# Kernel tuning notes

Hardware: AMD Instinct MI355X
Metric: run time of the kernel (lower is better)

## Reference

```python
import jax, jax.numpy as jnp
import numpy as np
from jax import lax

B, L, D_MODEL = 4, 1024, 512
D_STATE, D_CONV, D_INNER = 16, 4, 2 * D_MODEL


def setup_inputs() -> dict:
    key = jax.random.key(0)
    ks = jax.random.split(key, 8)
    s = 0.02
    x = jax.random.normal(ks[0], (B, L, D_MODEL), dtype=jnp.float32)
    W_in = jax.random.normal(ks[1], (D_MODEL, 2 * D_INNER), dtype=jnp.float32) * s
    conv_w = jax.random.normal(ks[2], (D_INNER, 1, D_CONV), dtype=jnp.float32) * s  # OIH, depthwise
    conv_b = jnp.zeros((D_INNER,), jnp.float32)
    W_x = jax.random.normal(ks[3], (D_INNER, 2 * D_STATE), dtype=jnp.float32) * s
    W_dt = jax.random.normal(ks[4], (D_INNER, D_INNER), dtype=jnp.float32) * s
    b_dt = jnp.zeros((D_INNER,), jnp.float32)
    # A_log = -logspace(log10(0.001), log10(1.0), d_state); used directly as A in the scan
    A_log = -jnp.logspace(np.log10(1e-3), 0.0, D_STATE, dtype=jnp.float32)
    D_skip = jnp.ones((D_INNER,), jnp.float32) * 0.1
    W_out = jax.random.normal(ks[5], (D_INNER, D_MODEL), dtype=jnp.float32) * s
    gamma = jnp.ones((D_MODEL,), jnp.float32)
    beta = jnp.zeros((D_MODEL,), jnp.float32)
    return dict(x=x, W_in=W_in, conv_w=conv_w, conv_b=conv_b, W_x=W_x, W_dt=W_dt,
                b_dt=b_dt, A_log=A_log, D_skip=D_skip, W_out=W_out, gamma=gamma, beta=beta)


def _mamba_forward(x, W_in, conv_w, conv_b, W_x, W_dt, b_dt, A_log, D_skip, W_out, gamma, beta):
    x = jnp.clip(x, -10.0, 10.0)
    x_and_res = x @ W_in                                  # [B, L, 2*d_inner]
    xp, res = jnp.split(x_and_res, 2, axis=-1)
    # Depthwise causal conv1d: torch pads d_conv-1 both sides then slices [:L] -> left-pad only.
    xt = jnp.transpose(xp, (0, 2, 1))                     # [B, d_inner, L]
    xc = lax.conv_general_dilated(xt, conv_w, window_strides=(1,),
                                  padding=[(D_CONV - 1, 0)],
                                  dimension_numbers=('NCH', 'OIH', 'NCH'),
                                  feature_group_count=D_INNER)
    xc = xc + conv_b[None, :, None]
    xc = jax.nn.silu(jnp.transpose(xc, (0, 2, 1)))        # [B, L, d_inner]
    ssm = xc @ W_x                                        # [B, L, 2*d_state]
    Bm, Cm = jnp.split(ssm, 2, axis=-1)                   # each [B, L, d_state]
    delta = xc @ W_dt + b_dt                              # [B, L, d_inner] (no softplus in source)

    # Selective scan over time (sequential recurrence)
    def step(h, inp):
        u_t, d_t, B_t, C_t = inp                          # [B,I], [B,I], [B,S], [B,S]
        dA = jnp.exp(jnp.clip(d_t[:, :, None] * A_log, -5.0, 5.0))   # [B, I, S]
        h = dA * h + (d_t[:, :, None] * B_t[:, None, :]) * u_t[:, :, None]
        y = jnp.einsum('bis,bs->bi', h, C_t)
        return h, y

    tm = lambda a: jnp.swapaxes(a, 0, 1)                  # time-major
    h0 = jnp.zeros((x.shape[0], D_INNER, D_STATE), xc.dtype)
    _, ys = lax.scan(step, h0, (tm(xc), tm(delta), tm(Bm), tm(Cm)))
    y = jnp.swapaxes(ys, 0, 1) + xc * D_skip              # D skip connection

    y = y * jax.nn.silu(res)                              # gating
    out = y @ W_out
    r = out + x                                           # residual
    mu = jnp.mean(r, axis=-1, keepdims=True)
    var = jnp.var(r, axis=-1, keepdims=True)
    return gamma * (r - mu) / jnp.sqrt(var + 1e-5) + beta


def reference(x, W_in, conv_w, conv_b, W_x, W_dt, b_dt, A_log, D_skip, W_out, gamma, beta):
    return _mamba_forward(x, W_in, conv_w, conv_b, W_x, W_dt, b_dt, A_log, D_skip, W_out, gamma, beta)
```

## Files before the change

kernel.cpp:

```cpp
#include <hip/hip_runtime.h>
#include <hip/hip_bf16.h>

typedef __hip_bfloat16 bf16;
typedef unsigned short ushort_t;
typedef unsigned int uint_t;
typedef __attribute__((ext_vector_type(8))) __bf16 bf16x8;
typedef __attribute__((ext_vector_type(8))) ushort_t u16x8;
typedef __attribute__((ext_vector_type(4))) ushort_t u16x4;
typedef __attribute__((ext_vector_type(4))) float f32x4;
typedef __attribute__((ext_vector_type(2))) float f32x2;

#define BB 4
#define LL 1024
#define DM 512
#define DS 16
#define DI 1024
#define ROWS 4096
#define NC 64
#define CT 16
#define NDTX 1152

__device__ __forceinline__ float b2f(bf16 v) { return __bfloat162float(v); }

__device__ __forceinline__ float load_flag(const void* src, int i, int isbf)
{
    return isbf ? b2f(((const bf16*)src)[i]) : ((const float*)src)[i];
}

__device__ __forceinline__ ushort_t f2b_bits(float v)
{
    bf16 t = __float2bfloat16(v);
    return *(ushort_t*)&t;
}

__device__ __forceinline__ float bits2f(ushort_t u)
{
    uint_t w = ((uint_t)u) << 16;
    return __uint_as_float(w);
}

__device__ __forceinline__ int detect_local(const ushort_t* wdt)
{
    __shared__ int bad;
    if (threadIdx.x == 0) bad = 0;
    __syncthreads();
    ushort_t u = wdt[threadIdx.x & 255];
    if (((u >> 7) & 0xFF) >= 127) atomicAdd(&bad, 1);
    __syncthreads();
    return (bad <= 8) ? 1 : 0;
}

__global__ __launch_bounds__(256)
void prep_all(const void* x, const void* Win, const void* Wdt, const void* Wx,
              const void* Wout, const void* cw, const void* cb, const void* Alog,
              const void* Dsk, const void* gam, const void* bet, const void* bdtin,
              bf16* __restrict__ xbf, bf16* __restrict__ WtIn,
              bf16* __restrict__ WtDtx, bf16* __restrict__ WtOut,
              float* __restrict__ ccw, float* __restrict__ ccb,
              float* __restrict__ cAlg, float* __restrict__ cDsk,
              float* __restrict__ cgam, float* __restrict__ cbet,
              float* __restrict__ bdtx)
{
    const int isbf = detect_local((const ushort_t*)Wdt);
    int blk = blockIdx.x;

    if (blk < 2048) {
        int idx = blk * 256 + threadIdx.x;
        float v[4];
        if (isbf) {
            uint2 raw = ((const uint2*)x)[idx];
            v[0] = __uint_as_float(raw.x << 16);
            v[1] = __uint_as_float(raw.x & 0xFFFF0000u);
            v[2] = __uint_as_float(raw.y << 16);
            v[3] = __uint_as_float(raw.y & 0xFFFF0000u);
        } else {
            float4 raw = ((const float4*)x)[idx];
            v[0] = raw.x; v[1] = raw.y; v[2] = raw.z; v[3] = raw.w;
        }
        uint_t b0, b1;
        b0 = f2b_bits(fminf(fmaxf(v[0], -10.f), 10.f))
           | ((uint_t)f2b_bits(fminf(fmaxf(v[1], -10.f), 10.f)) << 16);
        b1 = f2b_bits(fminf(fmaxf(v[2], -10.f), 10.f))
           | ((uint_t)f2b_bits(fminf(fmaxf(v[3], -10.f), 10.f)) << 16);
        uint2 ow; ow.x = b0; ow.y = b1;
        ((uint2*)xbf)[idx] = ow;
    } else if (blk < 4640) {
        int tb = blk - 2048;
        const void* src; bf16* dst; int K, Nsrc, tpr;
        if (tb < 1024)      { src = Win;  dst = WtIn;   K = 512;  Nsrc = 2048; tpr = 64; }
        else if (tb < 2048) { tb -= 1024; src = Wdt;  dst = WtDtx; K = 1024; Nsrc = 1024; tpr = 32; }
        else if (tb < 2080) { tb -= 2048; src = Wx;   dst = WtDtx + 1024 * 1024; K = 1024; Nsrc = 32; tpr = 1; }
        else                { tb -= 2080; src = Wout; dst = WtOut;  K = 1024; Nsrc = 512;  tpr = 16; }
        int k0 = (tb / tpr) * 32, n0 = (tb % tpr) * 32;

        __shared__ float tile[32][33];
        int tx = threadIdx.x & 31, ty = threadIdx.x >> 5;
        #pragma unroll
        for (int j = 0; j < 4; ++j)
            tile[ty + 8 * j][tx] = load_flag(src, (k0 + ty + 8 * j) * Nsrc + n0 + tx, isbf);
        __syncthreads();
        #pragma unroll
        for (int j = 0; j < 4; ++j)
            dst[(size_t)(n0 + ty + 8 * j) * K + k0 + tx] = __float2bfloat16(tile[tx][ty + 8 * j]);
    } else {
        int i = (blk - 4640) * 256 + threadIdx.x;
        if (i < 4096)        ccw[i] = load_flag(cw, i, isbf);
        else if (i < 5120)   ccb[i - 4096] = load_flag(cb, i - 4096, isbf);
        else if (i < 5136)   cAlg[i - 5120] = load_flag(Alog, i - 5120, isbf);
        else if (i < 6160)   cDsk[i - 5136] = load_flag(Dsk, i - 5136, isbf);
        else if (i < 6672)   cgam[i - 6160] = load_flag(gam, i - 6160, isbf);
        else if (i < 7184)   cbet[i - 6672] = load_flag(bet, i - 6672, isbf);
        else if (i < 8336) {
            int j = i - 7184;
            bdtx[j] = (j < DI) ? load_flag(bdtin, j, isbf) : 0.f;
        } else if (i < 106640) {
            (WtDtx + 1056 * 1024)[i - 8336] = __float2bfloat16(0.f);
        }
    }
}

__device__ __forceinline__ void gload16(const bf16* g, ushort_t* l)
{
    __builtin_amdgcn_global_load_lds(
        (const __attribute__((address_space(1))) void*)g,
        (__attribute__((address_space(3))) void*)l, 16, 0, 0);
}

template <int TM, int TN, bool OBF, bool OT, bool SPLIT>
__global__ __launch_bounds__(256)
void gemm_mfma(const bf16* __restrict__ A, const bf16* __restrict__ Bt,
               const float* __restrict__ bias, void* __restrict__ Cv,
               void* __restrict__ Cv2, int M, int N, int K)
{
    constexpr int MI = TM / 32, NJ = TN / 32;
    constexpr int NQA = TM * 8 / 256;
    constexpr int NQB = TN * 8 / 256;
    __shared__ ushort_t As[TM * 64];
    __shared__ ushort_t Bs[TN * 64];

    const int tid = threadIdx.x;
    const int lane = tid & 63;
    const int w = tid >> 6;
    const int wr = w >> 1, wc = w & 1;
    const int m0 = blockIdx.y * TM;
    const int n0 = blockIdx.x * TN;

    const bf16* gA[NQA]; ushort_t* lA[NQA];
    #pragma unroll
    for (int q = 0; q < NQA; ++q) {
        int p = q * 256 + tid;
        int row = p >> 3, kc = ((p & 7) - row) & 7;
        gA[q] = A + (size_t)(m0 + row) * K + kc * 8;
        lA[q] = &As[(q * 256 + w * 64) * 8];
    }
    const bf16* gB[NQB]; ushort_t* lB[NQB];
    #pragma unroll
    for (int q = 0; q < NQB; ++q) {
        int p = q * 256 + tid;
        int row = p >> 3, kc = ((p & 7) - row) & 7;
        gB[q] = Bt + (size_t)(n0 + row) * K + kc * 8;
        lB[q] = &Bs[(q * 256 + w * 64) * 8];
    }

    f32x4 acc[MI][NJ];
    #pragma unroll
    for (int i = 0; i < MI; ++i)
        #pragma unroll
        for (int j = 0; j < NJ; ++j)
            acc[i][j] = (f32x4){0.f, 0.f, 0.f, 0.f};

    const int ko = lane >> 4;
    const int ml = lane & 15;

    for (int k0 = 0; k0 < K; k0 += 64) {
        #pragma unroll
        for (int q = 0; q < NQA; ++q) gload16(gA[q] + k0, lA[q]);
        #pragma unroll
        for (int q = 0; q < NQB; ++q) gload16(gB[q] + k0, lB[q]);
        __syncthreads();

        #pragma unroll
        for (int half = 0; half < 2; ++half) {
            bf16x8 af[MI], bfr[NJ];
            #pragma unroll
            for (int i = 0; i < MI; ++i) {
                int m = wr * (TM / 2) + i * 16 + ml;
                af[i] = *(const bf16x8*)&As[(m * 8 + ((half * 4 + ko + m) & 7)) * 8];
            }
            #pragma unroll
            for (int j = 0; j < NJ; ++j) {
                int n = wc * (TN / 2) + j * 16 + ml;
                bfr[j] = *(const bf16x8*)&Bs[(n * 8 + ((half * 4 + ko + n) & 7)) * 8];
            }
            #pragma unroll
            for (int i = 0; i < MI; ++i)
                #pragma unroll
                for (int j = 0; j < NJ; ++j)
                    acc[i][j] = __builtin_amdgcn_mfma_f32_16x16x32_bf16(
                        af[i], bfr[j], acc[i][j], 0, 0, 0);
        }
        __syncthreads();
    }

    const int rq = lane >> 4;
    #pragma unroll
    for (int j = 0; j < NJ; ++j) {
        int n = n0 + wc * (TN / 2) + j * 16 + ml;
        float bv = bias ? bias[n] : 0.f;
        #pragma unroll
        for (int i = 0; i < MI; ++i) {
            int mb = m0 + wr * (TM / 2) + i * 16 + rq * 4;
            if (SPLIT && n >= 1024) {
                if (n < 1088) {
                    #pragma unroll
                    for (int r = 0; r < 4; ++r)
                        ((bf16*)Cv2)[(size_t)(mb + r) * 64 + (n - 1024)] =
                            __float2bfloat16(acc[i][j][r] + bv);
                }
            } else if (OT) {
                u16x4 pk;
                #pragma unroll
                for (int r = 0; r < 4; ++r)
                    pk[r] = f2b_bits(acc[i][j][r] + bv);
                *(u16x4*)((ushort_t*)Cv + (size_t)n * M + mb) = pk;
            } else {
                #pragma unroll
                for (int r = 0; r < 4; ++r) {
                    float v = acc[i][j][r] + bv;
                    if (OBF) ((bf16*)Cv)[(size_t)(mb + r) * N + n] = __float2bfloat16(v);
                    else     ((float*)Cv)[(size_t)(mb + r) * N + n] = v;
                }
            }
        }
    }
}

__global__ __launch_bounds__(256)
void conv_silu(const bf16* __restrict__ xrbT, const float* __restrict__ cw,
               const float* __restrict__ cb, bf16* __restrict__ xcT,
               bf16* __restrict__ xc)
{
    __shared__ ushort_t tile[64 * 72];
    const int blk = blockIdx.x;
    const int ch0 = (blk & 15) * 64;
    const int T0b = (blk >> 4) * 64;
    const int lc = threadIdx.x >> 2, tg = threadIdx.x & 3;
    const int i = ch0 + lc;
    const int T0 = T0b + tg * 16;

    const ushort_t* base = (const ushort_t*)xrbT + (size_t)i * ROWS + T0;
    u16x8 m0 = *(const u16x8*)base;
    u16x8 m1 = *(const u16x8*)(base + 8);
    u16x8 pv = {0, 0, 0, 0, 0, 0, 0, 0};
    if ((T0 & (LL - 1)) != 0) pv = *(const u16x8*)(base - 8);

    float4 w = ((const float4*)cw)[i];
    float bs = cb[i];
    float xm3 = bits2f(pv[5]), xm2 = bits2f(pv[6]), xm1 = bits2f(pv[7]);
    u16x8 o0, o1;
    #pragma unroll
    for (int tt = 0; tt < 16; ++tt) {
        float x0 = bits2f(tt < 8 ? m0[tt] : m1[tt - 8]);
        float acc = bs;
        acc = fmaf(xm3, w.x, acc);
        acc = fmaf(xm2, w.y, acc);
        acc = fmaf(xm1, w.z, acc);
        acc = fmaf(x0,  w.w, acc);
        ushort_t ob = f2b_bits(acc / (1.f + __expf(-acc)));
        if (tt < 8) o0[tt] = ob; else o1[tt - 8] = ob;
        xm3 = xm2; xm2 = xm1; xm1 = x0;
    }
    ushort_t* dt = (ushort_t*)xcT + (size_t)i * ROWS + T0;
    *(u16x8*)dt = o0;
    *(u16x8*)(dt + 8) = o1;
    *(u16x8*)&tile[lc * 72 + tg * 16] = o0;
    *(u16x8*)&tile[lc * 72 + tg * 16 + 8] = o1;
    __syncthreads();
    const int lt = threadIdx.x >> 2, cg = threadIdx.x & 3;
    u16x8 q0, q1;
    #pragma unroll
    for (int j = 0; j < 8; ++j) q0[j] = tile[(cg * 16 + j) * 72 + lt];
    #pragma unroll
    for (int j = 8; j < 16; ++j) q1[j - 8] = tile[(cg * 16 + j) * 72 + lt];
    ushort_t* wp = (ushort_t*)xc + (size_t)(T0b + lt) * DI + ch0 + cg * 16;
    *(u16x8*)wp = q0;
    *(u16x8*)(wp + 8) = q1;
}

__global__ __launch_bounds__(1024)
void scan_fused(const bf16* __restrict__ xcT, const bf16* __restrict__ dT,
                const bf16* __restrict__ ssm, const bf16* __restrict__ xrbT,
                const float* __restrict__ A_log, const float* __restrict__ Dskip,
                bf16* __restrict__ ybf)
{
    __shared__ uint_t lsum[DS * NC * 16];

    const int tid = threadIdx.x;
    const int b = blockIdx.x >> 6;
    const int ch0 = (blockIdx.x & 63) << 4;
    const int chl = tid & 15;
    const int c = tid >> 4;
    const int i = ch0 + chl;
    const size_t tb = (size_t)b * LL + c * CT;

    float a[DS];
    #pragma unroll
    for (int s = 0; s < DS; ++s) {
        uint_t bits = (uint_t)__builtin_amdgcn_readfirstlane((int)__float_as_uint(A_log[s]));
        a[s] = __uint_as_float(bits);
    }

    const u16x8* dp = (const u16x8*)((const ushort_t*)dT + (size_t)i * ROWS + tb);
    const u16x8* up = (const u16x8*)((const ushort_t*)xcT + (size_t)i * ROWS + tb);
    const u16x8* rp = (const u16x8*)((const ushort_t*)xrbT + (size_t)(1024 + i) * ROWS + tb);

    f32x2 h2[8], p2[8];
    #pragma unroll
    for (int k = 0; k < 8; ++k) {
        h2[k] = (f32x2){0.f, 0.f};
        p2[k] = (f32x2){1.f, 1.f};
    }

    #pragma unroll
    for (int half = 0; half < 2; ++half) {
        u16x8 dv8 = dp[half];
        u16x8 uv8 = up[half];
        #pragma unroll
        for (int t = 0; t < 8; ++t) {
            float dv = bits2f(dv8[t]);
            float uv = bits2f(uv8[t]);
            float du = dv * uv;
            f32x2 du2 = {du, du};
            const u16x8* sp = (const u16x8*)((const ushort_t*)ssm + (tb + half * 8 + t) * 64);
            u16x8 B0 = sp[0], B1 = sp[1];
            #pragma unroll
            for (int k = 0; k < 8; ++k) {
                float eA = fminf(fmaxf(dv * a[2 * k],     -5.f), 5.f);
                float eB = fminf(fmaxf(dv * a[2 * k + 1], -5.f), 5.f);
                f32x2 dA = {__expf(eA), __expf(eB)};
                f32x2 Bv = {bits2f(k < 4 ? B0[2 * k] : B1[2 * k - 8]),
                            bits2f(k < 4 ? B0[2 * k + 1] : B1[2 * k - 7])};
                h2[k] = dA * h2[k] + du2 * Bv;
                p2[k] = p2[k] * dA;
            }
        }
    }
    #pragma unroll
    for (int k = 0; k < 8; ++k) {
        lsum[(2 * k) * 1024 + tid] =
            (uint_t)f2b_bits(p2[k][0]) | ((uint_t)f2b_bits(h2[k][0]) << 16);
        lsum[(2 * k + 1) * 1024 + tid] =
            (uint_t)f2b_bits(p2[k][1]) | ((uint_t)f2b_bits(h2[k][1]) << 16);
    }
    __syncthreads();

    if (tid < 256) {
        int cl = tid & 15, s = tid >> 4;
        float hh = 0.f;
        for (int cc = 0; cc < NC; ++cc) {
            int off = s * 1024 + cc * 16 + cl;
            uint_t wrd = lsum[off];
            float pp = bits2f((ushort_t)(wrd & 0xFFFF));
            float qq = bits2f((ushort_t)(wrd >> 16));
            lsum[off] = (uint_t)f2b_bits(hh);
            hh = fmaf(pp, hh, qq);
        }
    }
    __syncthreads();

    #pragma unroll
    for (int k = 0; k < 8; ++k) {
        h2[k][0] = bits2f((ushort_t)lsum[(2 * k) * 1024 + tid]);
        h2[k][1] = bits2f((ushort_t)lsum[(2 * k + 1) * 1024 + tid]);
    }

    const float dsk = Dskip[i];

    #pragma unroll
    for (int half = 0; half < 2; ++half) {
        u16x8 dv8 = dp[half];
        u16x8 uv8 = up[half];
        u16x8 rv8 = rp[half];
        #pragma unroll
        for (int t = 0; t < 8; ++t) {
            float dv = bits2f(dv8[t]);
            float uv = bits2f(uv8[t]);
            float du = dv * uv;
            f32x2 du2 = {du, du};
            const u16x8* sp = (const u16x8*)((const ushort_t*)ssm + (tb + half * 8 + t) * 64);
            u16x8 B0 = sp[0], B1 = sp[1], C0 = sp[2], C1 = sp[3];
            f32x2 y2 = {0.f, 0.f};
            #pragma unroll
            for (int k = 0; k < 8; ++k) {
                float eA = fminf(fmaxf(dv * a[2 * k],     -5.f), 5.f);
                float eB = fminf(fmaxf(dv * a[2 * k + 1], -5.f), 5.f);
                f32x2 dA = {__expf(eA), __expf(eB)};
                f32x2 Bv = {bits2f(k < 4 ? B0[2 * k] : B1[2 * k - 8]),
                            bits2f(k < 4 ? B0[2 * k + 1] : B1[2 * k - 7])};
                f32x2 Cv = {bits2f(k < 4 ? C0[2 * k] : C1[2 * k - 8]),
                            bits2f(k < 4 ? C0[2 * k + 1] : C1[2 * k - 7])};
                h2[k] = dA * h2[k] + du2 * Bv;
                y2 = y2 + h2[k] * Cv;
            }
            float y = y2[0] + y2[1];
            float res = bits2f(rv8[t]);
            float g = res / (1.f + __expf(-res));
            ybf[(tb + half * 8 + t) * DI + i] = __float2bfloat16((y + uv * dsk) * g);
        }
    }
}

__global__ __launch_bounds__(256)
void ln_kernel(const bf16* __restrict__ outp, const void* __restrict__ xsrc,
               const void* __restrict__ wdt_probe,
               const float* __restrict__ gamma, const float* __restrict__ beta,
               void* __restrict__ out)
{
    const int isbf = detect_local((const ushort_t*)wdt_probe);
    const int row = blockIdx.x;
    const int tid = threadIdx.x;

    float r[2];
    float sum = 0.f, ss = 0.f;
    #pragma unroll
    for (int q = 0; q < 2; ++q) {
        int j = tid + q * 256;
        float xv = load_flag(xsrc, row * DM + j, isbf);
        xv = fminf(fmaxf(xv, -10.f), 10.f);
        float v = b2f(outp[(size_t)row * DM + j]) + xv;
        r[q] = v;
        sum += v;
        ss = fmaf(v, v, ss);
    }
    #pragma unroll
    for (int off = 32; off >= 1; off >>= 1) {
        sum += __shfl_down(sum, off);
        ss  += __shfl_down(ss, off);
    }
    __shared__ float s1[4], s2[4];
    __shared__ float stats[2];
    int wid = tid >> 6, lane = tid & 63;
    if (lane == 0) { s1[wid] = sum; s2[wid] = ss; }
    __syncthreads();
    if (tid == 0) {
        float S = s1[0] + s1[1] + s1[2] + s1[3];
        float Qq = s2[0] + s2[1] + s2[2] + s2[3];
        float mean = S / DM;
        float var = Qq / DM - mean * mean;
        stats[0] = mean;
        stats[1] = rsqrtf(var + 1e-5f);
    }
    __syncthreads();
    float mean = stats[0], rstd = stats[1];
    #pragma unroll
    for (int q = 0; q < 2; ++q) {
        int j = tid + q * 256;
        float v = (r[q] - mean) * rstd * gamma[j] + beta[j];
        size_t o = (size_t)row * DM + j;
        if (isbf) ((bf16*)out)[o] = __float2bfloat16(v);
        else      ((float*)out)[o] = v;
    }
}

extern "C" void kernel_launch(void* const* d_in, const int* in_sizes, int n_in,
                              void* d_out, int out_size, void* d_ws, size_t ws_size,
                              hipStream_t stream)
{
    float* W = (float*)d_ws;
    float* ccw  = W;
    float* ccb  = ccw  + 4096;
    float* cAlg = ccb  + 1024;
    float* cDsk = cAlg + 16;
    float* cgam = cDsk + 1024;
    float* cbet = cgam + 512;
    float* bdtx = cbet + 512;
    bf16*  xbf  = (bf16*)(bdtx + 1152);
    bf16*  xrbT = xbf  + 2097152;
    bf16*  xcT  = xrbT + 8388608;
    bf16*  xc   = xcT  + 4194304;
    bf16*  ybf  = xc   + 4194304;
    bf16*  dT   = ybf  + 4194304;
    bf16*  ssm  = dT   + 4194304;
    bf16*  outp = ssm  + 262144;
    bf16*  WtIn = outp + 2097152;
    bf16*  WtDtx= WtIn + 1048576;
    bf16*  WtOut= WtDtx+ 1179648;

    prep_all<<<5057, 256, 0, stream>>>(
        d_in[0], d_in[1], d_in[5], d_in[4], d_in[9], d_in[2], d_in[3],
        d_in[7], d_in[8], d_in[10], d_in[11], d_in[6],
        xbf, WtIn, WtDtx, WtOut, ccw, ccb, cAlg, cDsk, cgam, cbet, bdtx);

    gemm_mfma<128, 128, true, true, false><<<dim3(2048 / 128, ROWS / 128), 256, 0, stream>>>(
        xbf, WtIn, nullptr, xrbT, nullptr, ROWS, 2048, 512);

    conv_silu<<<1024, 256, 0, stream>>>(xrbT, ccw, ccb, xcT, xc);

    gemm_mfma<64, 128, true, true, true><<<dim3(NDTX / 128, ROWS / 64), 256, 0, stream>>>(
        xc, WtDtx, bdtx, dT, ssm, ROWS, NDTX, DI);

    scan_fused<<<256, 1024, 0, stream>>>(xcT, dT, ssm, xrbT, cAlg, cDsk, ybf);

    gemm_mfma<64, 64, true, false, false><<<dim3(DM / 64, ROWS / 64), 256, 0, stream>>>(
        ybf, WtOut, nullptr, outp, nullptr, ROWS, DM, DI);

    ln_kernel<<<ROWS, 256, 0, stream>>>(outp, d_in[0], d_in[5], cgam, cbet, d_out);
}
```

Baseline: 207.2 us.

## Halve scan chunk length, double block count, use exp2 with prescaled A

The selective-scan kernel now splits time into 128 chunks of 8 steps with 8 channels per block, so twice as many blocks run over the sequence and each thread's serial work is shorter. A_log is premultiplied by log2(e) in prep so that dA can use the hardware exp2 instruction directly, with the clamp bounds rescaled to match. The shared-memory carry buffer is XOR-swizzled to reduce bank conflicts. In exchange, the serial cross-chunk combine now runs 128 steps on only 128 threads, and launch_bounds requests higher occupancy, which may limit registers.

```diff
diff --git a/kernel.cpp b/kernel.cpp
--- a/kernel.cpp
+++ b/kernel.cpp
@@ -16,9 +16,11 @@
 #define DS 16
 #define DI 1024
 #define ROWS 4096
-#define NC 64
-#define CT 16
+#define NC 128
+#define CT 8
 #define NDTX 1152
+#define LOG2E 1.4426950408889634f
+#define ELIM 7.213475204444817f
 
 __device__ __forceinline__ float b2f(bf16 v) { return __bfloat162float(v); }
 
@@ -37,6 +39,17 @@
 {
     uint_t w = ((uint_t)u) << 16;
     return __uint_as_float(w);
+}
+
+__device__ __forceinline__ float exp2fast(float x)
+{
+#if __has_builtin(__builtin_amdgcn_exp2f)
+    return __builtin_amdgcn_exp2f(x);
+#else
+    float r;
+    asm("v_exp_f32 %0, %1" : "=v"(r) : "v"(x));
+    return r;
+#endif
 }
 
 __device__ __forceinline__ int detect_local(const ushort_t* wdt)
@@ -106,7 +119,7 @@
         int i = (blk - 4640) * 256 + threadIdx.x;
         if (i < 4096)        ccw[i] = load_flag(cw, i, isbf);
         else if (i < 5120)   ccb[i - 4096] = load_flag(cb, i - 4096, isbf);
-        else if (i < 5136)   cAlg[i - 5120] = load_flag(Alog, i - 5120, isbf);
+        else if (i < 5136)   cAlg[i - 5120] = load_flag(Alog, i - 5120, isbf) * LOG2E;
         else if (i < 6160)   cDsk[i - 5136] = load_flag(Dsk, i - 5136, isbf);
         else if (i < 6672)   cgam[i - 6160] = load_flag(gam, i - 6160, isbf);
         else if (i < 7184)   cbet[i - 6672] = load_flag(bet, i - 6672, isbf);
@@ -287,26 +300,26 @@
     *(u16x8*)(wp + 8) = q1;
 }
 
-__global__ __launch_bounds__(1024)
+__global__ __launch_bounds__(1024, 8)
 void scan_fused(const bf16* __restrict__ xcT, const bf16* __restrict__ dT,
                 const bf16* __restrict__ ssm, const bf16* __restrict__ xrbT,
-                const float* __restrict__ A_log, const float* __restrict__ Dskip,
+                const float* __restrict__ A_l2e, const float* __restrict__ Dskip,
                 bf16* __restrict__ ybf)
 {
-    __shared__ uint_t lsum[DS * NC * 16];
+    __shared__ uint_t lsum[DS * 1024];
 
     const int tid = threadIdx.x;
-    const int b = blockIdx.x >> 6;
-    const int ch0 = (blockIdx.x & 63) << 4;
-    const int chl = tid & 15;
-    const int c = tid >> 4;
+    const int b = blockIdx.x >> 7;
+    const int ch0 = (blockIdx.x & 127) << 3;
+    const int chl = tid & 7;
+    const int c = tid >> 3;
     const int i = ch0 + chl;
     const size_t tb = (size_t)b * LL + c * CT;
 
     float a[DS];
     #pragma unroll
     for (int s = 0; s < DS; ++s) {
-        uint_t bits = (uint_t)__builtin_amdgcn_readfirstlane((int)__float_as_uint(A_log[s]));
+        uint_t bits = (uint_t)__builtin_amdgcn_readfirstlane((int)__float_as_uint(A_l2e[s]));
         a[s] = __uint_as_float(bits);
     }
 
@@ -321,23 +334,24 @@
         p2[k] = (f32x2){1.f, 1.f};
     }
 
-    #pragma unroll
-    for (int half = 0; half < 2; ++half) {
-        u16x8 dv8 = dp[half];
-        u16x8 uv8 = up[half];
-        #pragma unroll
-        for (int t = 0; t < 8; ++t) {
+    {
+        u16x8 dv8 = dp[0];
+        u16x8 uv8 = up[0];
+        #pragma unroll
+        for (int t = 0; t < CT; ++t) {
             float dv = bits2f(dv8[t]);
             float uv = bits2f(uv8[t]);
             float du = dv * uv;
             f32x2 du2 = {du, du};
-            const u16x8* sp = (const u16x8*)((const ushort_t*)ssm + (tb + half * 8 + t) * 64);
+            f32x2 dv2 = {dv, dv};
+            const u16x8* sp = (const u16x8*)((const ushort_t*)ssm + (tb + t) * 64);
             u16x8 B0 = sp[0], B1 = sp[1];
             #pragma unroll
             for (int k = 0; k < 8; ++k) {
-                float eA = fminf(fmaxf(dv * a[2 * k],     -5.f), 5.f);
-                float eB = fminf(fmaxf(dv * a[2 * k + 1], -5.f), 5.f);
-                f32x2 dA = {__expf(eA), __expf(eB)};
+                f32x2 av = {a[2 * k], a[2 * k + 1]};
+                f32x2 e2 = dv2 * av;
+                f32x2 dA = {exp2fast(fminf(fmaxf(e2[0], -ELIM), ELIM)),
+                            exp2fast(fminf(fmaxf(e2[1], -ELIM), ELIM))};
                 f32x2 Bv = {bits2f(k < 4 ? B0[2 * k] : B1[2 * k - 8]),
                             bits2f(k < 4 ? B0[2 * k + 1] : B1[2 * k - 7])};
                 h2[k] = dA * h2[k] + du2 * Bv;
@@ -347,18 +361,20 @@
     }
     #pragma unroll
     for (int k = 0; k < 8; ++k) {
-        lsum[(2 * k) * 1024 + tid] =
+        int s0 = 2 * k, s1 = 2 * k + 1;
+        lsum[s0 * 1024 + (tid ^ ((s0 & 3) << 3))] =
             (uint_t)f2b_bits(p2[k][0]) | ((uint_t)f2b_bits(h2[k][0]) << 16);
-        lsum[(2 * k + 1) * 1024 + tid] =
+        lsum[s1 * 1024 + (tid ^ ((s1 & 3) << 3))] =
             (uint_t)f2b_bits(p2[k][1]) | ((uint_t)f2b_bits(h2[k][1]) << 16);
     }
     __syncthreads();
 
-    if (tid < 256) {
-        int cl = tid & 15, s = tid >> 4;
+    if (tid < 128) {
+        int cl = tid & 7, s = tid >> 3;
+        int sx = (s & 3) << 3;
         float hh = 0.f;
         for (int cc = 0; cc < NC; ++cc) {
-            int off = s * 1024 + cc * 16 + cl;
+            int off = s * 1024 + ((cc * 8 + cl) ^ sx);
             uint_t wrd = lsum[off];
             float pp = bits2f((ushort_t)(wrd & 0xFFFF));
             float qq = bits2f((ushort_t)(wrd >> 16));
@@ -370,31 +386,33 @@
 
     #pragma unroll
     for (int k = 0; k < 8; ++k) {
-        h2[k][0] = bits2f((ushort_t)lsum[(2 * k) * 1024 + tid]);
-        h2[k][1] = bits2f((ushort_t)lsum[(2 * k + 1) * 1024 + tid]);
+        int s0 = 2 * k, s1 = 2 * k + 1;
+        h2[k][0] = bits2f((ushort_t)lsum[s0 * 1024 + (tid ^ ((s0 & 3) << 3))]);
+        h2[k][1] = bits2f((ushort_t)lsum[s1 * 1024 + (tid ^ ((s1 & 3) << 3))]);
     }
 
     const float dsk = Dskip[i];
 
-    #pragma unroll
-    for (int half = 0; half < 2; ++half) {
-        u16x8 dv8 = dp[half];
-        u16x8 uv8 = up[half];
-        u16x8 rv8 = rp[half];
-        #pragma unroll
-        for (int t = 0; t < 8; ++t) {
+    {
+        u16x8 dv8 = dp[0];
+        u16x8 uv8 = up[0];
+        u16x8 rv8 = rp[0];
+        #pragma unroll
+        for (int t = 0; t < CT; ++t) {
             float dv = bits2f(dv8[t]);
             float uv = bits2f(uv8[t]);
             float du = dv * uv;
             f32x2 du2 = {du, du};
-            const u16x8* sp = (const u16x8*)((const ushort_t*)ssm + (tb + half * 8 + t) * 64);
+            f32x2 dv2 = {dv, dv};
+            const u16x8* sp = (const u16x8*)((const ushort_t*)ssm + (tb + t) * 64);
             u16x8 B0 = sp[0], B1 = sp[1], C0 = sp[2], C1 = sp[3];
             f32x2 y2 = {0.f, 0.f};
             #pragma unroll
             for (int k = 0; k < 8; ++k) {
-                float eA = fminf(fmaxf(dv * a[2 * k],     -5.f), 5.f);
-                float eB = fminf(fmaxf(dv * a[2 * k + 1], -5.f), 5.f);
-                f32x2 dA = {__expf(eA), __expf(eB)};
+                f32x2 av = {a[2 * k], a[2 * k + 1]};
+                f32x2 e2 = dv2 * av;
+                f32x2 dA = {exp2fast(fminf(fmaxf(e2[0], -ELIM), ELIM)),
+                            exp2fast(fminf(fmaxf(e2[1], -ELIM), ELIM))};
                 f32x2 Bv = {bits2f(k < 4 ? B0[2 * k] : B1[2 * k - 8]),
                             bits2f(k < 4 ? B0[2 * k + 1] : B1[2 * k - 7])};
                 f32x2 Cv = {bits2f(k < 4 ? C0[2 * k] : C1[2 * k - 8]),
@@ -405,7 +423,7 @@
             float y = y2[0] + y2[1];
             float res = bits2f(rv8[t]);
             float g = res / (1.f + __expf(-res));
-            ybf[(tb + half * 8 + t) * DI + i] = __float2bfloat16((y + uv * dsk) * g);
+            ybf[(tb + t) * DI + i] = __float2bfloat16((y + uv * dsk) * g);
         }
     }
 }
@@ -499,7 +517,7 @@
     gemm_mfma<64, 128, true, true, true><<<dim3(NDTX / 128, ROWS / 64), 256, 0, stream>>>(
         xc, WtDtx, bdtx, dT, ssm, ROWS, NDTX, DI);
 
-    scan_fused<<<256, 1024, 0, stream>>>(xcT, dT, ssm, xrbT, cAlg, cDsk, ybf);
+    scan_fused<<<512, 1024, 0, stream>>>(xcT, dT, ssm, xrbT, cAlg, cDsk, ybf);
 
     gemm_mfma<64, 64, true, false, false><<<dim3(DM / 64, ROWS / 64), 256, 0, stream>>>(
         ybf, WtOut, nullptr, outp, nullptr, ROWS, DM, DI);
```

After: 211.2 us. Within noise of the previous version (+1.9%).

## Decompose chunked scan output into local and carry-in terms using cumulative decay

Applied to the files above, without the earlier changes.

The chunked selective scan now computes the local output (with zero initial state) during the first pass, and stores it along with the cumulative delta per timestep. The second pass then only adds the carried-in state, weighted by exp2 of cumulative delta times A, so it no longer re-runs the recurrence or reloads B, delta and u. A is pre-scaled by log2(e) so the hardware exp2 instruction can be used, and the [-5,5] clamp on delta*A is dropped. The LDS layout is XOR-swizzled to avoid bank conflicts. The rewrite assumes the clamp never triggers and that the product of exponentials equals the exponential of the sum, which changes numerics wherever the clamp would have been active.

```diff
diff --git a/kernel.cpp b/kernel.cpp
--- a/kernel.cpp
+++ b/kernel.cpp
@@ -19,6 +19,7 @@
 #define NC 64
 #define CT 16
 #define NDTX 1152
+#define LOG2E 1.4426950408889634f
 
 __device__ __forceinline__ float b2f(bf16 v) { return __bfloat162float(v); }
 
@@ -37,6 +38,17 @@
 {
     uint_t w = ((uint_t)u) << 16;
     return __uint_as_float(w);
+}
+
+__device__ __forceinline__ float exp2fast(float x)
+{
+#if __has_builtin(__builtin_amdgcn_exp2f)
+    return __builtin_amdgcn_exp2f(x);
+#else
+    float r;
+    asm("v_exp_f32 %0, %1" : "=v"(r) : "v"(x));
+    return r;
+#endif
 }
 
 __device__ __forceinline__ int detect_local(const ushort_t* wdt)
@@ -106,7 +118,7 @@
         int i = (blk - 4640) * 256 + threadIdx.x;
         if (i < 4096)        ccw[i] = load_flag(cw, i, isbf);
         else if (i < 5120)   ccb[i - 4096] = load_flag(cb, i - 4096, isbf);
-        else if (i < 5136)   cAlg[i - 5120] = load_flag(Alog, i - 5120, isbf);
+        else if (i < 5136)   cAlg[i - 5120] = load_flag(Alog, i - 5120, isbf) * LOG2E;
         else if (i < 6160)   cDsk[i - 5136] = load_flag(Dsk, i - 5136, isbf);
         else if (i < 6672)   cgam[i - 6160] = load_flag(gam, i - 6160, isbf);
         else if (i < 7184)   cbet[i - 6672] = load_flag(bet, i - 6672, isbf);
@@ -290,10 +302,10 @@
 __global__ __launch_bounds__(1024)
 void scan_fused(const bf16* __restrict__ xcT, const bf16* __restrict__ dT,
                 const bf16* __restrict__ ssm, const bf16* __restrict__ xrbT,
-                const float* __restrict__ A_log, const float* __restrict__ Dskip,
+                const float* __restrict__ A_l2e, const float* __restrict__ Dskip,
                 bf16* __restrict__ ybf)
 {
-    __shared__ uint_t lsum[DS * NC * 16];
+    __shared__ uint_t lsum[DS * 1024];
 
     const int tid = threadIdx.x;
     const int b = blockIdx.x >> 6;
@@ -306,7 +318,7 @@
     float a[DS];
     #pragma unroll
     for (int s = 0; s < DS; ++s) {
-        uint_t bits = (uint_t)__builtin_amdgcn_readfirstlane((int)__float_as_uint(A_log[s]));
+        uint_t bits = (uint_t)__builtin_amdgcn_readfirstlane((int)__float_as_uint(A_l2e[s]));
         a[s] = __uint_as_float(bits);
     }
 
@@ -314,12 +326,15 @@
     const u16x8* up = (const u16x8*)((const ushort_t*)xcT + (size_t)i * ROWS + tb);
     const u16x8* rp = (const u16x8*)((const ushort_t*)xrbT + (size_t)(1024 + i) * ROWS + tb);
 
-    f32x2 h2[8], p2[8];
-    #pragma unroll
-    for (int k = 0; k < 8; ++k) {
-        h2[k] = (f32x2){0.f, 0.f};
-        p2[k] = (f32x2){1.f, 1.f};
-    }
+    const float dsk = Dskip[i];
+
+    f32x2 h2[8];
+    #pragma unroll
+    for (int k = 0; k < 8; ++k) h2[k] = (f32x2){0.f, 0.f};
+
+    float ylocal[CT];
+    float cumD[CT];
+    float cd = 0.f;
 
     #pragma unroll
     for (int half = 0; half < 2; ++half) {
@@ -327,38 +342,53 @@
         u16x8 uv8 = up[half];
         #pragma unroll
         for (int t = 0; t < 8; ++t) {
+            const int tt = half * 8 + t;
             float dv = bits2f(dv8[t]);
             float uv = bits2f(uv8[t]);
             float du = dv * uv;
+            cd += dv;
+            cumD[tt] = cd;
             f32x2 du2 = {du, du};
-            const u16x8* sp = (const u16x8*)((const ushort_t*)ssm + (tb + half * 8 + t) * 64);
-            u16x8 B0 = sp[0], B1 = sp[1];
+            f32x2 dv2 = {dv, dv};
+            const u16x8* sp = (const u16x8*)((const ushort_t*)ssm + (tb + tt) * 64);
+            u16x8 B0 = sp[0], B1 = sp[1], C0 = sp[2], C1 = sp[3];
+            f32x2 y2 = {0.f, 0.f};
             #pragma unroll
             for (int k = 0; k < 8; ++k) {
-                float eA = fminf(fmaxf(dv * a[2 * k],     -5.f), 5.f);
-                float eB = fminf(fmaxf(dv * a[2 * k + 1], -5.f), 5.f);
-                f32x2 dA = {__expf(eA), __expf(eB)};
+                f32x2 av = {a[2 * k], a[2 * k + 1]};
+                f32x2 e2 = dv2 * av;
+                f32x2 dA = {exp2fast(e2[0]), exp2fast(e2[1])};
                 f32x2 Bv = {bits2f(k < 4 ? B0[2 * k] : B1[2 * k - 8]),
                             bits2f(k < 4 ? B0[2 * k + 1] : B1[2 * k - 7])};
                 h2[k] = dA * h2[k] + du2 * Bv;
-                p2[k] = p2[k] * dA;
+                f32x2 Cv = {bits2f(k < 4 ? C0[2 * k] : C1[2 * k - 8]),
+                            bits2f(k < 4 ? C0[2 * k + 1] : C1[2 * k - 7])};
+                y2 = y2 + h2[k] * Cv;
             }
-        }
-    }
+            ylocal[tt] = y2[0] + y2[1] + uv * dsk;
+        }
+    }
+
+    f32x2 cdf = {cd, cd};
     #pragma unroll
     for (int k = 0; k < 8; ++k) {
-        lsum[(2 * k) * 1024 + tid] =
-            (uint_t)f2b_bits(p2[k][0]) | ((uint_t)f2b_bits(h2[k][0]) << 16);
-        lsum[(2 * k + 1) * 1024 + tid] =
-            (uint_t)f2b_bits(p2[k][1]) | ((uint_t)f2b_bits(h2[k][1]) << 16);
+        int s0 = 2 * k, s1 = 2 * k + 1;
+        f32x2 av = {a[s0], a[s1]};
+        f32x2 e2 = cdf * av;
+        f32x2 pc = {exp2fast(e2[0]), exp2fast(e2[1])};
+        lsum[s0 * 1024 + (tid ^ ((s0 & 1) << 4))] =
+            (uint_t)f2b_bits(pc[0]) | ((uint_t)f2b_bits(h2[k][0]) << 16);
+        lsum[s1 * 1024 + (tid ^ ((s1 & 1) << 4))] =
+            (uint_t)f2b_bits(pc[1]) | ((uint_t)f2b_bits(h2[k][1]) << 16);
     }
     __syncthreads();
 
     if (tid < 256) {
         int cl = tid & 15, s = tid >> 4;
+        int sx = (s & 1) << 4;
         float hh = 0.f;
         for (int cc = 0; cc < NC; ++cc) {
-            int off = s * 1024 + cc * 16 + cl;
+            int off = s * 1024 + ((cc * 16 + cl) ^ sx);
             uint_t wrd = lsum[off];
             float pp = bits2f((ushort_t)(wrd & 0xFFFF));
             float qq = bits2f((ushort_t)(wrd >> 16));
@@ -370,42 +400,34 @@
 
     #pragma unroll
     for (int k = 0; k < 8; ++k) {
-        h2[k][0] = bits2f((ushort_t)lsum[(2 * k) * 1024 + tid]);
-        h2[k][1] = bits2f((ushort_t)lsum[(2 * k + 1) * 1024 + tid]);
-    }
-
-    const float dsk = Dskip[i];
+        int s0 = 2 * k, s1 = 2 * k + 1;
+        h2[k][0] = bits2f((ushort_t)lsum[s0 * 1024 + (tid ^ ((s0 & 1) << 4))]);
+        h2[k][1] = bits2f((ushort_t)lsum[s1 * 1024 + (tid ^ ((s1 & 1) << 4))]);
+    }
 
     #pragma unroll
     for (int half = 0; half < 2; ++half) {
-        u16x8 dv8 = dp[half];
-        u16x8 uv8 = up[half];
         u16x8 rv8 = rp[half];
         #pragma unroll
         for (int t = 0; t < 8; ++t) {
-            float dv = bits2f(dv8[t]);
-            float uv = bits2f(uv8[t]);
-            float du = dv * uv;
-            f32x2 du2 = {du, du};
-            const u16x8* sp = (const u16x8*)((const ushort_t*)ssm + (tb + half * 8 + t) * 64);
-            u16x8 B0 = sp[0], B1 = sp[1], C0 = sp[2], C1 = sp[3];
+            const int tt = half * 8 + t;
+            const u16x8* sp = (const u16x8*)((const ushort_t*)ssm + (tb + tt) * 64);
+            u16x8 C0 = sp[2], C1 = sp[3];
+            f32x2 cd2 = {cumD[tt], cumD[tt]};
             f32x2 y2 = {0.f, 0.f};
             #pragma unroll
             for (int k = 0; k < 8; ++k) {
-                float eA = fminf(fmaxf(dv * a[2 * k],     -5.f), 5.f);
-                float eB = fminf(fmaxf(dv * a[2 * k + 1], -5.f), 5.f);
-                f32x2 dA = {__expf(eA), __expf(eB)};
-                f32x2 Bv = {bits2f(k < 4 ? B0[2 * k] : B1[2 * k - 8]),
-                            bits2f(k < 4 ? B0[2 * k + 1] : B1[2 * k - 7])};
+                f32x2 av = {a[2 * k], a[2 * k + 1]};
+                f32x2 e2 = cd2 * av;
+                f32x2 pt = {exp2fast(e2[0]), exp2fast(e2[1])};
                 f32x2 Cv = {bits2f(k < 4 ? C0[2 * k] : C1[2 * k - 8]),
                             bits2f(k < 4 ? C0[2 * k + 1] : C1[2 * k - 7])};
-                h2[k] = dA * h2[k] + du2 * Bv;
-                y2 = y2 + h2[k] * Cv;
+                y2 = y2 + (pt * h2[k]) * Cv;
             }
-            float y = y2[0] + y2[1];
+            float y = ylocal[tt] + y2[0] + y2[1];
             float res = bits2f(rv8[t]);
             float g = res / (1.f + __expf(-res));
-            ybf[(tb + half * 8 + t) * DI + i] = __float2bfloat16((y + uv * dsk) * g);
+            ybf[(tb + tt) * DI + i] = __float2bfloat16(y * g);
         }
     }
 }
```

Result: slower. 365.2 us (+76.2%).
